# Performance work log

Measured on AMD Instinct MI355X. Metric: run time of the kernel, lower is better.

Reference implementation:

```python
import jax, jax.numpy as jnp
import numpy as np

SCALES = (4, 8, 8)
PAD = 2
TOTAL = 256  # prod(SCALES) == frame shift
INDENT = PAD * TOTAL
BN_EPS = 1e-3  # keras BatchNormalization default


def _bn(x, g, b, m, v):
    return (x - m) * jax.lax.rsqrt(v + BN_EPS) * g + b


def _conv1d_valid(x, w):
    # x: [B, T, Cin], w: [K, Cin, Cout]
    return jax.lax.conv_general_dilated(x, w, (1,), 'VALID',
                                         dimension_numbers=('NWC', 'WIO', 'NWC'))


def _mel_conv_same(x, w):
    # per-mel-bin shared 1D conv along time. x: [B, T, M], w: [K]
    B, T, M = x.shape
    lhs = x.transpose(0, 2, 1).reshape(B * M, T, 1)
    rhs = w.reshape(-1, 1, 1)
    y = jax.lax.conv_general_dilated(lhs, rhs, (1,), 'SAME',
                                     dimension_numbers=('NWC', 'WIO', 'NWC'))
    return y.reshape(B, M, T).transpose(0, 2, 1)


def _gru(x, Wx, Wh, bx, bh):
    # keras GRUCell (reset_after=True): gate order z, r, h; h' = z*h + (1-z)*hh
    xp = x @ Wx + bx  # [B, T, 3H], input projection hoisted out of the scan
    H = Wh.shape[0]
    h0 = jnp.zeros((x.shape[0], H), x.dtype)

    def step(h, xt):
        rp = h @ Wh + bh
        xz, xr, xh = jnp.split(xt, 3, axis=-1)
        rz, rr, rh = jnp.split(rp, 3, axis=-1)
        z = jax.nn.sigmoid(xz + rz)
        r = jax.nn.sigmoid(xr + rr)
        hh = jnp.tanh(xh + r * rh)
        hn = z * h + (1.0 - z) * hh
        return hn, hn

    _, ys = jax.lax.scan(step, h0, xp.transpose(1, 0, 2))
    return ys.transpose(1, 0, 2)


def setup_inputs() -> dict:
    key = jax.random.key(0)
    ks = iter(jax.random.split(key, 64))
    B, T_MEL, M, C, H, R = 4, 44, 80, 128, 512, 10
    T_UP = TOTAL * (T_MEL - 2 * PAD)  # 10240
    s = 0.05
    d = {}
    d['audios'] = jax.random.normal(next(ks), (B, T_UP + 1), jnp.float32)
    d['mels'] = jax.random.normal(next(ks), (B, T_MEL, M), jnp.float32)
    d['w_mel0'] = jnp.full((2 * SCALES[0] + 1,), 1.0 / (2 * SCALES[0] + 1), jnp.float32)
    d['w_mel1'] = jnp.full((2 * SCALES[1] + 1,), 1.0 / (2 * SCALES[1] + 1), jnp.float32)
    d['w_mel2'] = jnp.full((2 * SCALES[2] + 1,), 1.0 / (2 * SCALES[2] + 1), jnp.float32)
    d['mr_conv0_w'] = jax.random.normal(next(ks), (5, M, C), jnp.float32) * s
    d['mr_bn0_g'] = jax.random.uniform(next(ks), (C,), jnp.float32, 0.5, 1.5)
    d['mr_bn0_b'] = jax.random.normal(next(ks), (C,), jnp.float32) * s
    d['mr_bn0_m'] = jnp.zeros((C,), jnp.float32)
    d['mr_bn0_v'] = jnp.ones((C,), jnp.float32)
    d['r_w1'] = jax.random.normal(next(ks), (R, C, C), jnp.float32) * s
    d['r_bn1_g'] = jax.random.uniform(next(ks), (R, C), jnp.float32, 0.5, 1.5)
    d['r_bn1_b'] = jax.random.normal(next(ks), (R, C), jnp.float32) * s
    d['r_bn1_m'] = jnp.zeros((R, C), jnp.float32)
    d['r_bn1_v'] = jnp.ones((R, C), jnp.float32)
    d['r_w2'] = jax.random.normal(next(ks), (R, C, C), jnp.float32) * s
    d['r_bn2_g'] = jax.random.uniform(next(ks), (R, C), jnp.float32, 0.5, 1.5)
    d['r_bn2_b'] = jax.random.normal(next(ks), (R, C), jnp.float32) * s
    d['r_bn2_m'] = jnp.zeros((R, C), jnp.float32)
    d['r_bn2_v'] = jnp.ones((R, C), jnp.float32)
    d['mr_out_w'] = jax.random.normal(next(ks), (C, C), jnp.float32) * s
    d['mr_out_b'] = jnp.zeros((C,), jnp.float32)
    A4 = C // 4  # 32
    d['Wi'] = jax.random.normal(next(ks), (1 + M + A4, H), jnp.float32) * s
    d['bi'] = jnp.zeros((H,), jnp.float32)
    d['Wx0'] = jax.random.normal(next(ks), (H, 3 * H), jnp.float32) * s
    d['Wh0'] = jax.random.normal(next(ks), (H, 3 * H), jnp.float32) * s
    d['bx0'] = jnp.zeros((3 * H,), jnp.float32)
    d['bh0'] = jnp.zeros((3 * H,), jnp.float32)
    d['Wx1'] = jax.random.normal(next(ks), (H + A4, 3 * H), jnp.float32) * s
    d['Wh1'] = jax.random.normal(next(ks), (H, 3 * H), jnp.float32) * s
    d['bx1'] = jnp.zeros((3 * H,), jnp.float32)
    d['bh1'] = jnp.zeros((3 * H,), jnp.float32)
    d['Wd0'] = jax.random.normal(next(ks), (H + A4, H), jnp.float32) * s
    d['bd0'] = jnp.zeros((H,), jnp.float32)
    d['Wd1'] = jax.random.normal(next(ks), (H + A4, H), jnp.float32) * s
    d['bd1'] = jnp.zeros((H,), jnp.float32)
    d['Wp'] = jax.random.normal(next(ks), (H, 30), jnp.float32) * s
    d['bp'] = jnp.zeros((30,), jnp.float32)
    return d


def reference(audios, mels, w_mel0, w_mel1, w_mel2,
              mr_conv0_w, mr_bn0_g, mr_bn0_b, mr_bn0_m, mr_bn0_v,
              r_w1, r_bn1_g, r_bn1_b, r_bn1_m, r_bn1_v,
              r_w2, r_bn2_g, r_bn2_b, r_bn2_m, r_bn2_v,
              mr_out_w, mr_out_b, Wi, bi,
              Wx0, Wh0, bx0, bh0, Wx1, Wh1, bx1, bh1,
              Wd0, bd0, Wd1, bd1, Wp, bp):
    # ---- UpsampleNet mel branch: nearest upsample + smoothing conv per scale ----
    x = mels
    for w, scale in zip((w_mel0, w_mel1, w_mel2), SCALES):
        x = jnp.repeat(x, scale, axis=1)
        x = _mel_conv_same(x, w)
    mels_up = x[:, INDENT:-INDENT, :]  # [B, T_up, 80]

    # ---- UpsampleNet aux branch: MelResNet (inference BN) + nearest upsample ----
    a = jax.nn.relu(_bn(_conv1d_valid(mels, mr_conv0_w),
                        mr_bn0_g, mr_bn0_b, mr_bn0_m, mr_bn0_v))
    for i in range(r_w1.shape[0]):
        y = jax.nn.relu(_bn(a @ r_w1[i], r_bn1_g[i], r_bn1_b[i], r_bn1_m[i], r_bn1_v[i]))
        y = _bn(y @ r_w2[i], r_bn2_g[i], r_bn2_b[i], r_bn2_m[i], r_bn2_v[i])
        a = a + y
    a = a @ mr_out_w + mr_out_b
    aux = jnp.repeat(a, TOTAL, axis=1)  # [B, T_up, 128]
    a0, a1, a2, a3 = jnp.split(aux, 4, axis=-1)

    # ---- WaveRNN teacher-forced trunk ----
    x = jnp.concatenate([audios[:, :-1, None], mels_up, a0], axis=-1)
    x = x @ Wi + bi  # [B, T_up, 512]
    x = _gru(x, Wx0, Wh0, bx0, bh0) + x
    x = _gru(jnp.concatenate([x, a1], axis=-1), Wx1, Wh1, bx1, bh1) + x
    x = jax.nn.relu(jnp.concatenate([x, a2], axis=-1) @ Wd0 + bd0) + x
    x = jax.nn.relu(jnp.concatenate([x, a3], axis=-1) @ Wd1 + bd1) + x
    logits = x @ Wp + bp  # [B, T_up, 30] (MoL parameters)
    return logits
```

## Files before the change

kernel.cpp:

```cpp
#include <hip/hip_runtime.h>
#include <hip/hip_bf16.h>

#define T_SEQ 10240
#define GRU_W 8

typedef short bf16x8 __attribute__((ext_vector_type(8)));
typedef float f32x4 __attribute__((ext_vector_type(4)));

__device__ __forceinline__ float bf2f(unsigned short u) {
    return __uint_as_float(((unsigned int)u) << 16);
}

__global__ void upsample_kernel(const float* __restrict__ in, float* __restrict__ out,
                                const float* __restrict__ wk,
                                int B, int Tin, int Tout, int shift, int taps)
{
    int idx = blockIdx.x * blockDim.x + threadIdx.x;
    int total = B * Tout * 80;
    if (idx >= total) return;
    int m = idx % 80;
    int r = idx / 80;
    int t = r % Tout;
    int b = r / Tout;
    int s = taps >> 1;
    float acc = 0.f;
    for (int d = -s; d <= s; ++d) {
        int i = t + d;
        if (i >= 0 && i < Tout)
            acc += in[((size_t)b * Tin + (i >> shift)) * 80 + m] * wk[d + s];
    }
    out[idx] = acc;
}

__global__ __launch_bounds__(128) void conv0_kernel(
    const float* __restrict__ mels, const float* __restrict__ w,
    const float* __restrict__ g, const float* __restrict__ b,
    const float* __restrict__ m_, const float* __restrict__ v_,
    float* __restrict__ a)
{
    __shared__ float xin[400];
    int bt = blockIdx.x;
    int bb = bt / 40, t = bt % 40;
    int c = threadIdx.x;
    for (int idx = c; idx < 400; idx += 128)
        xin[idx] = mels[((size_t)bb * 44 + t + idx / 80) * 80 + (idx % 80)];
    __syncthreads();
    float s = 0.f;
    for (int q = 0; q < 400; ++q) s += xin[q] * w[q * 128 + c];
    s = (s - m_[c]) * rsqrtf(v_[c] + 1e-3f) * g[c] + b[c];
    a[bt * 128 + c] = fmaxf(s, 0.f);
}

__global__ __launch_bounds__(128) void resblock_kernel(
    const float* __restrict__ W1, const float* __restrict__ W2,
    const float* __restrict__ g1, const float* __restrict__ b1,
    const float* __restrict__ m1, const float* __restrict__ v1,
    const float* __restrict__ g2, const float* __restrict__ b2,
    const float* __restrict__ m2, const float* __restrict__ v2,
    float* __restrict__ a)
{
    __shared__ float ain[128], y1[128];
    int tok = blockIdx.x;
    int c = threadIdx.x;
    ain[c] = a[tok * 128 + c];
    __syncthreads();
    float s = 0.f;
    #pragma unroll 8
    for (int k = 0; k < 128; ++k) s += ain[k] * W1[k * 128 + c];
    s = (s - m1[c]) * rsqrtf(v1[c] + 1e-3f) * g1[c] + b1[c];
    y1[c] = fmaxf(s, 0.f);
    __syncthreads();
    float s2 = 0.f;
    #pragma unroll 8
    for (int k = 0; k < 128; ++k) s2 += y1[k] * W2[k * 128 + c];
    s2 = (s2 - m2[c]) * rsqrtf(v2[c] + 1e-3f) * g2[c] + b2[c];
    a[tok * 128 + c] = ain[c] + s2;
}

__global__ __launch_bounds__(128) void outmat_kernel(
    const float* __restrict__ W, const float* __restrict__ bias,
    const float* __restrict__ a, float* __restrict__ out)
{
    __shared__ float ain[128];
    int tok = blockIdx.x;
    int c = threadIdx.x;
    ain[c] = a[tok * 128 + c];
    __syncthreads();
    float s = 0.f;
    #pragma unroll 8
    for (int k = 0; k < 128; ++k) s += ain[k] * W[k * 128 + c];
    out[tok * 128 + c] = s + bias[c];
}

__device__ __forceinline__ float fetchA(int mode, int row, int k, int K,
    const float* audio, const float* melsup, const float* cond, const float* xA)
{
    if (k >= K) return 0.f;
    int b = row / T_SEQ;
    int t = row - b * T_SEQ;
    if (mode == 0) {
        if (k == 0) return audio[(size_t)b * (T_SEQ + 1) + t];
        if (k < 81) return melsup[((size_t)b * 11264 + 512 + t) * 80 + (k - 1)];
        return cond[((size_t)b * 40 + (t >> 8)) * 128 + (k - 81)];
    }
    if (k < 512) return xA[(size_t)row * 512 + k];
    int co = (mode == 2) ? 32 : (mode == 3) ? 64 : 96;
    return cond[((size_t)b * 40 + (t >> 8)) * 128 + co + (k - 512)];
}

__global__ __launch_bounds__(256) void gemm_big(
    int mode, int N, int K,
    const float* __restrict__ W, const float* __restrict__ bias1,
    const float* __restrict__ bias2,
    const float* __restrict__ audio, const float* __restrict__ melsup,
    const float* __restrict__ cond, const float* __restrict__ xA,
    const float* __restrict__ resid, float* __restrict__ outF,
    __hip_bfloat16* __restrict__ outB)
{
    __shared__ float As[16][68];
    __shared__ float Bs[16][68];
    const int tid = threadIdx.x;
    const int row0 = blockIdx.y * 64;
    const int col0 = blockIdx.x * 64;
    const int tx = tid & 15, ty = tid >> 4;
    float acc[4][4] = {};
    const int nkt = (K + 15) >> 4;
    for (int kt = 0; kt < nkt; ++kt) {
        const int kb = kt << 4;
        #pragma unroll
        for (int l = 0; l < 4; ++l) {
            int k = (tid >> 6) + l * 4;
            int m = tid & 63;
            float bv = 0.f;
            if (kb + k < K) bv = W[(size_t)(kb + k) * N + col0 + m];
            Bs[k][m] = bv;
        }
        if (mode != 0) {
            int m = tid >> 2, kq = tid & 3;
            int row = row0 + m;
            int k = kb + kq * 4;
            if (k + 3 < 512) {
                float4 v = *reinterpret_cast<const float4*>(xA + (size_t)row * 512 + k);
                As[kq * 4 + 0][m] = v.x; As[kq * 4 + 1][m] = v.y;
                As[kq * 4 + 2][m] = v.z; As[kq * 4 + 3][m] = v.w;
            } else {
                #pragma unroll
                for (int i = 0; i < 4; ++i)
                    As[kq * 4 + i][m] = fetchA(mode, row, k + i, K, audio, melsup, cond, xA);
            }
        } else {
            #pragma unroll
            for (int l = 0; l < 4; ++l) {
                int k = (tid >> 6) + l * 4;
                int m = tid & 63;
                As[k][m] = fetchA(0, row0 + m, kb + k, K, audio, melsup, cond, xA);
            }
        }
        __syncthreads();
        #pragma unroll
        for (int k = 0; k < 16; ++k) {
            float a0 = As[k][(ty << 2) + 0], a1 = As[k][(ty << 2) + 1];
            float a2 = As[k][(ty << 2) + 2], a3 = As[k][(ty << 2) + 3];
            float b0 = Bs[k][(tx << 2) + 0], b1 = Bs[k][(tx << 2) + 1];
            float b2 = Bs[k][(tx << 2) + 2], b3 = Bs[k][(tx << 2) + 3];
            acc[0][0] += a0 * b0; acc[0][1] += a0 * b1; acc[0][2] += a0 * b2; acc[0][3] += a0 * b3;
            acc[1][0] += a1 * b0; acc[1][1] += a1 * b1; acc[1][2] += a1 * b2; acc[1][3] += a1 * b3;
            acc[2][0] += a2 * b0; acc[2][1] += a2 * b1; acc[2][2] += a2 * b2; acc[2][3] += a2 * b3;
            acc[3][0] += a3 * b0; acc[3][1] += a3 * b1; acc[3][2] += a3 * b2; acc[3][3] += a3 * b3;
        }
        __syncthreads();
    }
    #pragma unroll
    for (int i = 0; i < 4; ++i) {
        int row = row0 + (ty << 2) + i;
        #pragma unroll
        for (int jt = 0; jt < 4; ++jt) {
            int col = col0 + (tx << 2) + jt;
            float v = acc[i][jt] + bias1[col];
            if (bias2 && col < 1024) v += bias2[col];
            if (mode == 0) {
                outF[(size_t)row * N + col] = v;
            } else if (mode <= 2) {
                outB[(size_t)row * 1536 + col] = __float2bfloat16(v);
            } else {
                v = fmaxf(v, 0.f) + resid[(size_t)row * 512 + col];
                outF[(size_t)row * 512 + col] = v;
            }
        }
    }
}

__global__ __launch_bounds__(256) void pack_wh_kernel(const float* __restrict__ Wh,
                                                      unsigned short* __restrict__ out)
{
    int gid = blockIdx.x * 256 + threadIdx.x;
    int l = gid & 63;
    int idx = gid >> 6;
    int kt = idx & 15; idx >>= 4;
    int ntL = idx & 1; idx >>= 1;
    int w = idx % 6;
    int wg = idx / 6;
    int nt = 2 * w + ntL;
    int g = nt >> 2, u = nt & 3;
    int n = g * 512 + wg * 64 + u * 16 + (l & 15);
    int k0 = kt * 32 + (l >> 4) * 8;
    unsigned short* dst = out + (size_t)gid * 8;
    #pragma unroll
    for (int i = 0; i < 8; ++i) {
        __hip_bfloat16 hv = __float2bfloat16(Wh[(size_t)(k0 + i) * 1536 + n]);
        dst[i] = *reinterpret_cast<unsigned short*>(&hv);
    }
}

__global__ __launch_bounds__(512, 2) void gru_mfma8(
    const unsigned short* __restrict__ wpack,
    const float* __restrict__ bh,
    const __hip_bfloat16* __restrict__ xp,
    float* __restrict__ xio,
    unsigned int* __restrict__ hpair,
    int T)
{
    __shared__ alignas(16) unsigned short h_sh[16 * 512];
    __shared__ alignas(16) unsigned short xp_sh[2][4][3][64];
    __shared__ alignas(8)  float xv_sh[2][4][64];
    __shared__ alignas(16) float acc_sh[12][16][4];

    const int tid = threadIdx.x;
    const int wg = blockIdx.x;
    const int w = tid >> 6;
    const int l = tid & 63;

    {
        uint4* z = reinterpret_cast<uint4*>(h_sh);
        z[tid] = make_uint4(0, 0, 0, 0);
        z[tid + 512] = make_uint4(0, 0, 0, 0);
    }

    bf16x8 wf[2][16];
    if (w < 6) {
        const bf16x8* wp = reinterpret_cast<const bf16x8*>(wpack);
        const int base = (wg * 6 + w) * 2 * 16 * 64;
        #pragma unroll
        for (int n = 0; n < 2; ++n)
            #pragma unroll
            for (int kt = 0; kt < 16; ++kt)
                wf[n][kt] = wp[base + (n * 16 + kt) * 64 + l];
    }

    float bhh = 0.f, hprev = 0.f;
    if (tid < 256) bhh = bh[1024 + wg * 64 + (tid & 63)];

    if (tid < 128) {
        for (int z = tid; z < 192; z += 128) {
            int bg = z >> 4, s = z & 15;
            int b = bg / 3, g = bg % 3;
            unsigned long long v = *reinterpret_cast<const unsigned long long*>(
                reinterpret_cast<const unsigned short*>(xp) +
                (size_t)(b * T) * 1536 + g * 512 + wg * 64 + s * 4);
            *reinterpret_cast<unsigned long long*>(&xp_sh[0][b][g][s * 4]) = v;
        }
        int b = tid >> 5, pr = tid & 31;
        float2 v = *reinterpret_cast<const float2*>(
            xio + (size_t)(b * T) * 512 + wg * 64 + pr * 2);
        *reinterpret_cast<float2*>(&xv_sh[0][b][pr * 2]) = v;
    }
    __syncthreads();

    const unsigned long long* hp64 = reinterpret_cast<const unsigned long long*>(hpair);

    for (int t = 0; t < T; ++t) {
        const int cur = t & 1, nxt = cur ^ 1;

        const unsigned long long* src = hp64 + (size_t)cur * 1024 + tid * 2;
        const unsigned tg = (unsigned)t & 0xffffu;
        unsigned long long u0 = __hip_atomic_load(src + 0, __ATOMIC_RELAXED, __HIP_MEMORY_SCOPE_AGENT);
        unsigned long long u1 = __hip_atomic_load(src + 1, __ATOMIC_RELAXED, __HIP_MEMORY_SCOPE_AGENT);
        while ((((unsigned)(u0 >> 16) & 0xffffu) != tg) | ((unsigned)(u0 >> 48) != tg) |
               (((unsigned)(u1 >> 16) & 0xffffu) != tg) | ((unsigned)(u1 >> 48) != tg)) {
            __builtin_amdgcn_s_sleep(1);
            u0 = __hip_atomic_load(src + 0, __ATOMIC_RELAXED, __HIP_MEMORY_SCOPE_AGENT);
            u1 = __hip_atomic_load(src + 1, __ATOMIC_RELAXED, __HIP_MEMORY_SCOPE_AGENT);
        }
        {
            const int pb = tid >> 7;
            const int j0 = (tid * 4) & 511;
            unsigned long long wv =
                (u0 & 0xffffull) | ((u0 >> 32) & 0xffffull) << 16 |
                (u1 & 0xffffull) << 32 | ((u1 >> 32) & 0xffffull) << 48;
            const int chunk = (j0 >> 3) ^ (pb & 7);
            *reinterpret_cast<unsigned long long*>(
                reinterpret_cast<char*>(h_sh) + pb * 1024 + chunk * 16 + (j0 & 7) * 2) = wv;
        }
        __syncthreads();

        if (w >= 6 && t + 1 < T) {
            int t6 = tid - 384;
            for (int z = t6; z < 192; z += 128) {
                int bg = z >> 4, s = z & 15;
                int b = bg / 3, g = bg % 3;
                unsigned long long v = *reinterpret_cast<const unsigned long long*>(
                    reinterpret_cast<const unsigned short*>(xp) +
                    (size_t)(b * T + t + 1) * 1536 + g * 512 + wg * 64 + s * 4);
                *reinterpret_cast<unsigned long long*>(&xp_sh[nxt][b][g][s * 4]) = v;
            }
            int b = t6 >> 5, pr = t6 & 31;
            float2 v = *reinterpret_cast<const float2*>(
                xio + (size_t)(b * T + t + 1) * 512 + wg * 64 + pr * 2);
            *reinterpret_cast<float2*>(&xv_sh[nxt][b][pr * 2]) = v;
        }

        if (w < 6) {
            f32x4 acc0 = {0, 0, 0, 0}, acc1 = {0, 0, 0, 0};
            const int rb = l & 15, q = l >> 4;
            #pragma unroll
            for (int kt = 0; kt < 16; ++kt) {
                bf16x8 afr = *reinterpret_cast<const bf16x8*>(
                    reinterpret_cast<const char*>(h_sh) + rb * 1024 +
                    ((((kt * 4 + q) ^ (rb & 7))) << 4));
                acc0 = __builtin_amdgcn_mfma_f32_16x16x32_bf16(afr, wf[0][kt], acc0, 0, 0, 0);
                acc1 = __builtin_amdgcn_mfma_f32_16x16x32_bf16(afr, wf[1][kt], acc1, 0, 0, 0);
            }
            if (l < 16) {
                *reinterpret_cast<f32x4*>(&acc_sh[2 * w][l][0]) = acc0;
                *reinterpret_cast<f32x4*>(&acc_sh[2 * w + 1][l][0]) = acc1;
            }
        }
        __syncthreads();

        if (tid < 256) {
            const int b = tid >> 6, jl = tid & 63, j = wg * 64 + jl;
            const int u = jl >> 4, n16 = jl & 15;
            float az = acc_sh[u][n16][b];
            float ar = acc_sh[4 + u][n16][b];
            float ah = acc_sh[8 + u][n16][b];
            float xz = bf2f(xp_sh[cur][b][0][jl]);
            float xr = bf2f(xp_sh[cur][b][1][jl]);
            float xh = bf2f(xp_sh[cur][b][2][jl]);
            float xv = xv_sh[cur][b][jl];
            float z = 1.f / (1.f + __expf(-(xz + az)));
            float r = 1.f / (1.f + __expf(-(xr + ar)));
            float e2 = __expf(-2.f * (xh + r * (ah + bhh)));
            float hh = (1.f - e2) / (1.f + e2);
            float hn = z * hprev + (1.f - z) * hh;
            hprev = hn;
            __hip_bfloat16 hb16 = __float2bfloat16(hn);
            unsigned hv = ((unsigned)((t + 1) & 0xffff) << 16) |
                          (unsigned)*reinterpret_cast<unsigned short*>(&hb16);
            __hip_atomic_store(hpair + (size_t)nxt * 2048 + b * 512 + j, hv,
                               __ATOMIC_RELAXED, __HIP_MEMORY_SCOPE_AGENT);
            xio[(size_t)(b * T + t) * 512 + j] = xv + hn;
        }
    }
}

__global__ __launch_bounds__(256) void wp_kernel(
    const float* __restrict__ x, const float* __restrict__ Wp,
    const float* __restrict__ bp, float* __restrict__ out)
{
    int r = threadIdx.x >> 5, c = threadIdx.x & 31;
    size_t row = (size_t)blockIdx.x * 8 + r;
    if (c >= 30) return;
    const float* xr = x + row * 512;
    float acc = 0.f;
    #pragma unroll 8
    for (int k = 0; k < 512; ++k) acc += xr[k] * Wp[k * 30 + c];
    out[row * 30 + c] = acc + bp[c];
}

extern "C" void kernel_launch(void* const* d_in, const int* in_sizes, int n_in,
                              void* d_out, int out_size, void* d_ws, size_t ws_size,
                              hipStream_t stream)
{
    const float* audios = (const float*)d_in[0];
    const float* mels   = (const float*)d_in[1];
    const float* w_mel0 = (const float*)d_in[2];
    const float* w_mel1 = (const float*)d_in[3];
    const float* w_mel2 = (const float*)d_in[4];
    const float* conv0w = (const float*)d_in[5];
    const float* bn0g = (const float*)d_in[6];
    const float* bn0b = (const float*)d_in[7];
    const float* bn0m = (const float*)d_in[8];
    const float* bn0v = (const float*)d_in[9];
    const float* r_w1   = (const float*)d_in[10];
    const float* r_bn1g = (const float*)d_in[11];
    const float* r_bn1b = (const float*)d_in[12];
    const float* r_bn1m = (const float*)d_in[13];
    const float* r_bn1v = (const float*)d_in[14];
    const float* r_w2   = (const float*)d_in[15];
    const float* r_bn2g = (const float*)d_in[16];
    const float* r_bn2b = (const float*)d_in[17];
    const float* r_bn2m = (const float*)d_in[18];
    const float* r_bn2v = (const float*)d_in[19];
    const float* mr_out_w = (const float*)d_in[20];
    const float* mr_out_b = (const float*)d_in[21];
    const float* Wi = (const float*)d_in[22];
    const float* bi = (const float*)d_in[23];
    const float* Wx0 = (const float*)d_in[24];
    const float* Wh0 = (const float*)d_in[25];
    const float* bx0 = (const float*)d_in[26];
    const float* bh0 = (const float*)d_in[27];
    const float* Wx1 = (const float*)d_in[28];
    const float* Wh1 = (const float*)d_in[29];
    const float* bx1 = (const float*)d_in[30];
    const float* bh1 = (const float*)d_in[31];
    const float* Wd0 = (const float*)d_in[32];
    const float* bd0 = (const float*)d_in[33];
    const float* Wd1 = (const float*)d_in[34];
    const float* bd1 = (const float*)d_in[35];
    const float* Wp = (const float*)d_in[36];
    const float* bp = (const float*)d_in[37];

    char* ws = (char*)d_ws;
    size_t off = 0;
    auto alloc = [&](size_t n) { size_t r = off; off += (n + 255) & ~(size_t)255; return r; };
    const size_t M = 4 * (size_t)T_SEQ;
    size_t xp_off = alloc(M * 1536 * 2);
    size_t x_off  = alloc(M * 512 * 4);
    size_t s1_off = alloc((size_t)4 * 176 * 80 * 4);
    size_t s2_off = alloc((size_t)4 * 1408 * 80 * 4);
    size_t s3_off = alloc((size_t)4 * 11264 * 80 * 4);
    size_t ca_off = alloc((size_t)160 * 128 * 4);
    size_t cf_off = alloc((size_t)160 * 128 * 4);
    size_t wp0_off = alloc((size_t)98304 * 8 * 2);
    size_t wp1_off = alloc((size_t)98304 * 8 * 2);
    size_t hp_off  = alloc(2 * 2048 * 4);

    __hip_bfloat16* xp = (__hip_bfloat16*)(ws + xp_off);
    float* x3   = (float*)(ws + xp_off);
    float* xbuf = (float*)(ws + x_off);
    float* st1  = (float*)(ws + s1_off);
    float* st2  = (float*)(ws + s2_off);
    float* st3  = (float*)(ws + s3_off);
    float* conda = (float*)(ws + ca_off);
    float* condf = (float*)(ws + cf_off);
    unsigned short* wpack0 = (unsigned short*)(ws + wp0_off);
    unsigned short* wpack1 = (unsigned short*)(ws + wp1_off);
    unsigned int* hpair = (unsigned int*)(ws + hp_off);
    float* outp = (float*)d_out;

    pack_wh_kernel<<<384, 256, 0, stream>>>(Wh0, wpack0);
    pack_wh_kernel<<<384, 256, 0, stream>>>(Wh1, wpack1);

    {
        int tot1 = 4 * 176 * 80;
        upsample_kernel<<<(tot1 + 255) / 256, 256, 0, stream>>>(mels, st1, w_mel0, 4, 44, 176, 2, 9);
        int tot2 = 4 * 1408 * 80;
        upsample_kernel<<<(tot2 + 255) / 256, 256, 0, stream>>>(st1, st2, w_mel1, 4, 176, 1408, 3, 17);
        int tot3 = 4 * 11264 * 80;
        upsample_kernel<<<(tot3 + 255) / 256, 256, 0, stream>>>(st2, st3, w_mel2, 4, 1408, 11264, 3, 17);
    }
    conv0_kernel<<<160, 128, 0, stream>>>(mels, conv0w, bn0g, bn0b, bn0m, bn0v, conda);
    for (int i = 0; i < 10; ++i) {
        resblock_kernel<<<160, 128, 0, stream>>>(
            r_w1 + (size_t)i * 128 * 128, r_w2 + (size_t)i * 128 * 128,
            r_bn1g + i * 128, r_bn1b + i * 128, r_bn1m + i * 128, r_bn1v + i * 128,
            r_bn2g + i * 128, r_bn2b + i * 128, r_bn2m + i * 128, r_bn2v + i * 128,
            conda);
    }
    outmat_kernel<<<160, 128, 0, stream>>>(mr_out_w, mr_out_b, conda, condf);

    dim3 blk(256);
    gemm_big<<<dim3(8, 640), blk, 0, stream>>>(0, 512, 113, Wi, bi, nullptr,
        audios, st3, condf, nullptr, nullptr, xbuf, nullptr);
    gemm_big<<<dim3(24, 640), blk, 0, stream>>>(1, 1536, 512, Wx0, bx0, bh0,
        nullptr, nullptr, condf, xbuf, nullptr, nullptr, xp);
    hipMemsetAsync(ws + hp_off, 0, 2 * 2048 * 4, stream);
    gru_mfma8<<<GRU_W, 512, 0, stream>>>(wpack0, bh0, xp, xbuf, hpair, T_SEQ);
    gemm_big<<<dim3(24, 640), blk, 0, stream>>>(2, 1536, 544, Wx1, bx1, bh1,
        nullptr, nullptr, condf, xbuf, nullptr, nullptr, xp);
    hipMemsetAsync(ws + hp_off, 0, 2 * 2048 * 4, stream);
    gru_mfma8<<<GRU_W, 512, 0, stream>>>(wpack1, bh1, xp, xbuf, hpair, T_SEQ);
    gemm_big<<<dim3(8, 640), blk, 0, stream>>>(3, 512, 544, Wd0, bd0, nullptr,
        nullptr, nullptr, condf, xbuf, xbuf, x3, nullptr);
    gemm_big<<<dim3(8, 640), blk, 0, stream>>>(4, 512, 544, Wd1, bd1, nullptr,
        nullptr, nullptr, condf, x3, x3, xbuf, nullptr);
    wp_kernel<<<5120, 256, 0, stream>>>(xbuf, Wp, bp, outp);
}
```

Before: 47.59 ms.

## Move dense GEMMs to bf16 MFMA and deepen GRU input staging pipeline

Replaces the fp32 SIMT GEMM for the GRU input projections and the two dense layers with a bf16 MFMA kernel that uses pre-transposed, padded bf16 weight copies. The goal is to cut the time spent in these large matmuls. The GRU recurrence kernel also changes: it uses a 3-slot staging buffer with a register-held prefetch two steps ahead, and 16-byte hidden-state polling loads done by half of the threads. The trade-offs are extra bf16 rounding of the activations and weights, plus more packing kernels at startup.

```diff
diff --git a/kernel.cpp b/kernel.cpp
--- a/kernel.cpp
+++ b/kernel.cpp
@@ -9,6 +9,10 @@
 
 __device__ __forceinline__ float bf2f(unsigned short u) {
     return __uint_as_float(((unsigned int)u) << 16);
+}
+__device__ __forceinline__ unsigned short f2bf(float f) {
+    __hip_bfloat16 h = __float2bfloat16(f);
+    return *reinterpret_cast<unsigned short*>(&h);
 }
 
 __global__ void upsample_kernel(const float* __restrict__ in, float* __restrict__ out,
@@ -92,30 +96,11 @@
     out[tok * 128 + c] = s + bias[c];
 }
 
-__device__ __forceinline__ float fetchA(int mode, int row, int k, int K,
-    const float* audio, const float* melsup, const float* cond, const float* xA)
-{
-    if (k >= K) return 0.f;
-    int b = row / T_SEQ;
-    int t = row - b * T_SEQ;
-    if (mode == 0) {
-        if (k == 0) return audio[(size_t)b * (T_SEQ + 1) + t];
-        if (k < 81) return melsup[((size_t)b * 11264 + 512 + t) * 80 + (k - 1)];
-        return cond[((size_t)b * 40 + (t >> 8)) * 128 + (k - 81)];
-    }
-    if (k < 512) return xA[(size_t)row * 512 + k];
-    int co = (mode == 2) ? 32 : (mode == 3) ? 64 : 96;
-    return cond[((size_t)b * 40 + (t >> 8)) * 128 + co + (k - 512)];
-}
-
 __global__ __launch_bounds__(256) void gemm_big(
-    int mode, int N, int K,
+    int N, int K,
     const float* __restrict__ W, const float* __restrict__ bias1,
-    const float* __restrict__ bias2,
     const float* __restrict__ audio, const float* __restrict__ melsup,
-    const float* __restrict__ cond, const float* __restrict__ xA,
-    const float* __restrict__ resid, float* __restrict__ outF,
-    __hip_bfloat16* __restrict__ outB)
+    const float* __restrict__ cond, float* __restrict__ outF)
 {
     __shared__ float As[16][68];
     __shared__ float Bs[16][68];
@@ -134,27 +119,17 @@
             float bv = 0.f;
             if (kb + k < K) bv = W[(size_t)(kb + k) * N + col0 + m];
             Bs[k][m] = bv;
-        }
-        if (mode != 0) {
-            int m = tid >> 2, kq = tid & 3;
             int row = row0 + m;
-            int k = kb + kq * 4;
-            if (k + 3 < 512) {
-                float4 v = *reinterpret_cast<const float4*>(xA + (size_t)row * 512 + k);
-                As[kq * 4 + 0][m] = v.x; As[kq * 4 + 1][m] = v.y;
-                As[kq * 4 + 2][m] = v.z; As[kq * 4 + 3][m] = v.w;
-            } else {
-                #pragma unroll
-                for (int i = 0; i < 4; ++i)
-                    As[kq * 4 + i][m] = fetchA(mode, row, k + i, K, audio, melsup, cond, xA);
-            }
-        } else {
-            #pragma unroll
-            for (int l = 0; l < 4; ++l) {
-                int k = (tid >> 6) + l * 4;
-                int m = tid & 63;
-                As[k][m] = fetchA(0, row0 + m, kb + k, K, audio, melsup, cond, xA);
-            }
+            int b = row / T_SEQ;
+            int t = row - b * T_SEQ;
+            int kk = kb + k;
+            float av = 0.f;
+            if (kk < K) {
+                if (kk == 0) av = audio[(size_t)b * (T_SEQ + 1) + t];
+                else if (kk < 81) av = melsup[((size_t)b * 11264 + 512 + t) * 80 + (kk - 1)];
+                else av = cond[((size_t)b * 40 + (t >> 8)) * 128 + (kk - 81)];
+            }
+            As[k][m] = av;
         }
         __syncthreads();
         #pragma unroll
@@ -176,15 +151,120 @@
         #pragma unroll
         for (int jt = 0; jt < 4; ++jt) {
             int col = col0 + (tx << 2) + jt;
-            float v = acc[i][jt] + bias1[col];
-            if (bias2 && col < 1024) v += bias2[col];
-            if (mode == 0) {
-                outF[(size_t)row * N + col] = v;
-            } else if (mode <= 2) {
-                outB[(size_t)row * 1536 + col] = __float2bfloat16(v);
+            outF[(size_t)row * N + col] = acc[i][jt] + bias1[col];
+        }
+    }
+}
+
+__global__ __launch_bounds__(256) void pack_wt_kernel(const float* __restrict__ W,
+                                                      unsigned short* __restrict__ out,
+                                                      int K, int N)
+{
+    int idx = blockIdx.x * 256 + threadIdx.x;
+    if (idx >= N * 576) return;
+    int n = idx / 576, kp = idx % 576;
+    out[idx] = (kp < K) ? f2bf(W[(size_t)kp * N + n]) : (unsigned short)0;
+}
+
+__global__ __launch_bounds__(256) void gemm_mfma(
+    int mode, int K,
+    const unsigned short* __restrict__ Wt,
+    const float* __restrict__ bias1,
+    const float* __restrict__ bias2,
+    const float* __restrict__ cond,
+    const float* __restrict__ xA,
+    const float* __restrict__ resid,
+    float* __restrict__ outF,
+    __hip_bfloat16* __restrict__ outB)
+{
+    __shared__ alignas(16) unsigned short A_sh[64][72];
+    __shared__ alignas(16) unsigned short B_sh[128][72];
+    const int tid = threadIdx.x;
+    const int row0 = blockIdx.y * 64;
+    const int col0 = blockIdx.x * 128;
+    const int wv = tid >> 6, l = tid & 63;
+
+    f32x4 acc[4][2] = {};
+    const int nkt = (K + 63) >> 6;
+    for (int it = 0; it < nkt; ++it) {
+        const int kb = it << 6;
+        {
+            const int r = tid >> 2, q = tid & 3;
+            const int row = row0 + r;
+            unsigned short tmp[16];
+            if (kb + 64 <= 512) {
+                const float* src = xA + (size_t)row * 512 + kb + q * 16;
+                #pragma unroll
+                for (int e = 0; e < 16; e += 4) {
+                    float4 v = *reinterpret_cast<const float4*>(src + e);
+                    tmp[e + 0] = f2bf(v.x); tmp[e + 1] = f2bf(v.y);
+                    tmp[e + 2] = f2bf(v.z); tmp[e + 3] = f2bf(v.w);
+                }
             } else {
-                v = fmaxf(v, 0.f) + resid[(size_t)row * 512 + col];
-                outF[(size_t)row * 512 + col] = v;
+                const int b = row / T_SEQ, trow = row - b * T_SEQ;
+                const int co = (mode == 2) ? 32 : (mode == 3) ? 64 : 96;
+                const float* cp = cond + ((size_t)b * 40 + (trow >> 8)) * 128 + co;
+                #pragma unroll
+                for (int e = 0; e < 16; ++e) {
+                    int k = kb + q * 16 + e;
+                    float v = 0.f;
+                    if (k < 512) v = xA[(size_t)row * 512 + k];
+                    else if (k < K) v = cp[k - 512];
+                    tmp[e] = f2bf(v);
+                }
+            }
+            #pragma unroll
+            for (int e = 0; e < 16; e += 8)
+                *reinterpret_cast<uint4*>(&A_sh[r][q * 16 + e]) =
+                    *reinterpret_cast<const uint4*>(&tmp[e]);
+        }
+        {
+            const int c = tid >> 1, half = tid & 1;
+            const unsigned short* src = Wt + (size_t)(col0 + c) * 576 + kb + half * 32;
+            #pragma unroll
+            for (int e = 0; e < 32; e += 8)
+                *reinterpret_cast<uint4*>(&B_sh[c][half * 32 + e]) =
+                    *reinterpret_cast<const uint4*>(src + e);
+        }
+        __syncthreads();
+        const int rsel = l & 15, q = l >> 4;
+        #pragma unroll
+        for (int ks = 0; ks < 2; ++ks) {
+            bf16x8 a[4], b[2];
+            #pragma unroll
+            for (int mf = 0; mf < 4; ++mf)
+                a[mf] = *reinterpret_cast<const bf16x8*>(
+                    &A_sh[mf * 16 + rsel][ks * 32 + q * 8]);
+            #pragma unroll
+            for (int nf = 0; nf < 2; ++nf)
+                b[nf] = *reinterpret_cast<const bf16x8*>(
+                    &B_sh[wv * 32 + nf * 16 + rsel][ks * 32 + q * 8]);
+            #pragma unroll
+            for (int mf = 0; mf < 4; ++mf)
+                #pragma unroll
+                for (int nf = 0; nf < 2; ++nf)
+                    acc[mf][nf] = __builtin_amdgcn_mfma_f32_16x16x32_bf16(
+                        a[mf], b[nf], acc[mf][nf], 0, 0, 0);
+        }
+        __syncthreads();
+    }
+    const int rsel = l & 15, q = l >> 4;
+    #pragma unroll
+    for (int mf = 0; mf < 4; ++mf) {
+        #pragma unroll
+        for (int nf = 0; nf < 2; ++nf) {
+            #pragma unroll
+            for (int i = 0; i < 4; ++i) {
+                int row = row0 + mf * 16 + q * 4 + i;
+                int col = col0 + wv * 32 + nf * 16 + rsel;
+                float v = acc[mf][nf][i] + bias1[col];
+                if (mode <= 2) {
+                    if (col < 1024) v += bias2[col];
+                    outB[(size_t)row * 1536 + col] = __float2bfloat16(v);
+                } else {
+                    v = fmaxf(v, 0.f) + resid[(size_t)row * 512 + col];
+                    outF[(size_t)row * 512 + col] = v;
+                }
             }
         }
     }
@@ -206,10 +286,8 @@
     int k0 = kt * 32 + (l >> 4) * 8;
     unsigned short* dst = out + (size_t)gid * 8;
     #pragma unroll
-    for (int i = 0; i < 8; ++i) {
-        __hip_bfloat16 hv = __float2bfloat16(Wh[(size_t)(k0 + i) * 1536 + n]);
-        dst[i] = *reinterpret_cast<unsigned short*>(&hv);
-    }
+    for (int i = 0; i < 8; ++i)
+        dst[i] = f2bf(Wh[(size_t)(k0 + i) * 1536 + n]);
 }
 
 __global__ __launch_bounds__(512, 2) void gru_mfma8(
@@ -221,8 +299,8 @@
     int T)
 {
     __shared__ alignas(16) unsigned short h_sh[16 * 512];
-    __shared__ alignas(16) unsigned short xp_sh[2][4][3][64];
-    __shared__ alignas(8)  float xv_sh[2][4][64];
+    __shared__ alignas(16) unsigned short xp_sh[3][4][3][64];
+    __shared__ alignas(16) float xv_sh[3][4][64];
     __shared__ alignas(16) float acc_sh[12][16][4];
 
     const int tid = threadIdx.x;
@@ -232,8 +310,7 @@
 
     {
         uint4* z = reinterpret_cast<uint4*>(h_sh);
-        z[tid] = make_uint4(0, 0, 0, 0);
-        z[tid + 512] = make_uint4(0, 0, 0, 0);
+        for (int i = tid; i < 1024; i += 512) z[i] = make_uint4(0, 0, 0, 0);
     }
 
     bf16x8 wf[2][16];
@@ -250,64 +327,79 @@
     float bhh = 0.f, hprev = 0.f;
     if (tid < 256) bhh = bh[1024 + wg * 64 + (tid & 63)];
 
-    if (tid < 128) {
-        for (int z = tid; z < 192; z += 128) {
-            int bg = z >> 4, s = z & 15;
-            int b = bg / 3, g = bg % 3;
-            unsigned long long v = *reinterpret_cast<const unsigned long long*>(
-                reinterpret_cast<const unsigned short*>(xp) +
-                (size_t)(b * T) * 1536 + g * 512 + wg * 64 + s * 4);
-            *reinterpret_cast<unsigned long long*>(&xp_sh[0][b][g][s * 4]) = v;
-        }
-        int b = tid >> 5, pr = tid & 31;
-        float2 v = *reinterpret_cast<const float2*>(
-            xio + (size_t)(b * T) * 512 + wg * 64 + pr * 2);
-        *reinterpret_cast<float2*>(&xv_sh[0][b][pr * 2]) = v;
+    const int xc = tid - 384;
+    uint4 hold_a = make_uint4(0, 0, 0, 0), hold_b = make_uint4(0, 0, 0, 0);
+    #define STAGE_LOAD(c, t, dstv)                                              \
+        { int c_ = (c);                                                         \
+          if (c_ < 96) { int g_ = c_ / 32, b_ = (c_ % 32) / 8, s_ = c_ % 8;     \
+            dstv = *reinterpret_cast<const uint4*>(                             \
+                reinterpret_cast<const unsigned short*>(xp) +                   \
+                ((size_t)b_ * T + (t)) * 1536 + g_ * 512 + wg * 64 + s_ * 8);   \
+          } else { int d_ = c_ - 96, b_ = d_ >> 4, s_ = d_ & 15;                \
+            dstv = *reinterpret_cast<const uint4*>(                             \
+                xio + ((size_t)b_ * T + (t)) * 512 + wg * 64 + s_ * 4); } }
+    #define STAGE_WRITE(c, buf, v)                                              \
+        { int c_ = (c);                                                         \
+          if (c_ < 96) { int g_ = c_ / 32, b_ = (c_ % 32) / 8, s_ = c_ % 8;     \
+            *reinterpret_cast<uint4*>(&xp_sh[buf][b_][g_][s_ * 8]) = v;         \
+          } else { int d_ = c_ - 96, b_ = d_ >> 4, s_ = d_ & 15;                \
+            *reinterpret_cast<uint4*>(&xv_sh[buf][b_][s_ * 4]) = v; } }
+
+    if (w >= 6) {
+        uint4 v;
+        STAGE_LOAD(xc, 0, v); STAGE_WRITE(xc, 0, v);
+        if (xc < 32) { STAGE_LOAD(128 + xc, 0, v); STAGE_WRITE(128 + xc, 0, v); }
+        if (T > 1) {
+            STAGE_LOAD(xc, 1, hold_a);
+            if (xc < 32) STAGE_LOAD(128 + xc, 1, hold_b);
+        }
     }
     __syncthreads();
 
     const unsigned long long* hp64 = reinterpret_cast<const unsigned long long*>(hpair);
+    const int pb = tid >> 6;
+    const int pchunk = (tid & 63) ^ (pb & 7);
 
     for (int t = 0; t < T; ++t) {
-        const int cur = t & 1, nxt = cur ^ 1;
-
-        const unsigned long long* src = hp64 + (size_t)cur * 1024 + tid * 2;
-        const unsigned tg = (unsigned)t & 0xffffu;
-        unsigned long long u0 = __hip_atomic_load(src + 0, __ATOMIC_RELAXED, __HIP_MEMORY_SCOPE_AGENT);
-        unsigned long long u1 = __hip_atomic_load(src + 1, __ATOMIC_RELAXED, __HIP_MEMORY_SCOPE_AGENT);
-        while ((((unsigned)(u0 >> 16) & 0xffffu) != tg) | ((unsigned)(u0 >> 48) != tg) |
-               (((unsigned)(u1 >> 16) & 0xffffu) != tg) | ((unsigned)(u1 >> 48) != tg)) {
-            __builtin_amdgcn_s_sleep(1);
-            u0 = __hip_atomic_load(src + 0, __ATOMIC_RELAXED, __HIP_MEMORY_SCOPE_AGENT);
-            u1 = __hip_atomic_load(src + 1, __ATOMIC_RELAXED, __HIP_MEMORY_SCOPE_AGENT);
-        }
-        {
-            const int pb = tid >> 7;
-            const int j0 = (tid * 4) & 511;
-            unsigned long long wv =
-                (u0 & 0xffffull) | ((u0 >> 32) & 0xffffull) << 16 |
-                (u1 & 0xffffull) << 32 | ((u1 >> 32) & 0xffffull) << 48;
-            const int chunk = (j0 >> 3) ^ (pb & 7);
-            *reinterpret_cast<unsigned long long*>(
-                reinterpret_cast<char*>(h_sh) + pb * 1024 + chunk * 16 + (j0 & 7) * 2) = wv;
+        const int cur = t & 1;
+        const int bu = t % 3;
+
+        if (tid < 256) {
+            const unsigned long long* src = hp64 + (size_t)cur * 1024 + tid * 4;
+            const unsigned tg = (unsigned)t & 0xffffu;
+            unsigned long long u0 = __hip_atomic_load(src + 0, __ATOMIC_RELAXED, __HIP_MEMORY_SCOPE_AGENT);
+            unsigned long long u1 = __hip_atomic_load(src + 1, __ATOMIC_RELAXED, __HIP_MEMORY_SCOPE_AGENT);
+            unsigned long long u2 = __hip_atomic_load(src + 2, __ATOMIC_RELAXED, __HIP_MEMORY_SCOPE_AGENT);
+            unsigned long long u3 = __hip_atomic_load(src + 3, __ATOMIC_RELAXED, __HIP_MEMORY_SCOPE_AGENT);
+            while ((((unsigned)(u0 >> 16) & 0xffffu) != tg) | ((unsigned)(u0 >> 48) != tg) |
+                   (((unsigned)(u1 >> 16) & 0xffffu) != tg) | ((unsigned)(u1 >> 48) != tg) |
+                   (((unsigned)(u2 >> 16) & 0xffffu) != tg) | ((unsigned)(u2 >> 48) != tg) |
+                   (((unsigned)(u3 >> 16) & 0xffffu) != tg) | ((unsigned)(u3 >> 48) != tg)) {
+                __builtin_amdgcn_s_sleep(1);
+                u0 = __hip_atomic_load(src + 0, __ATOMIC_RELAXED, __HIP_MEMORY_SCOPE_AGENT);
+                u1 = __hip_atomic_load(src + 1, __ATOMIC_RELAXED, __HIP_MEMORY_SCOPE_AGENT);
+                u2 = __hip_atomic_load(src + 2, __ATOMIC_RELAXED, __HIP_MEMORY_SCOPE_AGENT);
+                u3 = __hip_atomic_load(src + 3, __ATOMIC_RELAXED, __HIP_MEMORY_SCOPE_AGENT);
+            }
+            uint4 wv;
+            wv.x = (unsigned)(u0 & 0xffffull) | ((unsigned)((u0 >> 32) & 0xffffull) << 16);
+            wv.y = (unsigned)(u1 & 0xffffull) | ((unsigned)((u1 >> 32) & 0xffffull) << 16);
+            wv.z = (unsigned)(u2 & 0xffffull) | ((unsigned)((u2 >> 32) & 0xffffull) << 16);
+            wv.w = (unsigned)(u3 & 0xffffull) | ((unsigned)((u3 >> 32) & 0xffffull) << 16);
+            *reinterpret_cast<uint4*>(
+                reinterpret_cast<char*>(h_sh) + pb * 1024 + pchunk * 16) = wv;
+        } else if (w >= 6) {
+            if (t + 1 < T) {
+                const int bn = (t + 1) % 3;
+                STAGE_WRITE(xc, bn, hold_a);
+                if (xc < 32) STAGE_WRITE(128 + xc, bn, hold_b);
+            }
+            if (t + 2 < T) {
+                STAGE_LOAD(xc, t + 2, hold_a);
+                if (xc < 32) STAGE_LOAD(128 + xc, t + 2, hold_b);
+            }
         }
         __syncthreads();
-
-        if (w >= 6 && t + 1 < T) {
-            int t6 = tid - 384;
-            for (int z = t6; z < 192; z += 128) {
-                int bg = z >> 4, s = z & 15;
-                int b = bg / 3, g = bg % 3;
-                unsigned long long v = *reinterpret_cast<const unsigned long long*>(
-                    reinterpret_cast<const unsigned short*>(xp) +
-                    (size_t)(b * T + t + 1) * 1536 + g * 512 + wg * 64 + s * 4);
-                *reinterpret_cast<unsigned long long*>(&xp_sh[nxt][b][g][s * 4]) = v;
-            }
-            int b = t6 >> 5, pr = t6 & 31;
-            float2 v = *reinterpret_cast<const float2*>(
-                xio + (size_t)(b * T + t + 1) * 512 + wg * 64 + pr * 2);
-            *reinterpret_cast<float2*>(&xv_sh[nxt][b][pr * 2]) = v;
-        }
 
         if (w < 6) {
             f32x4 acc0 = {0, 0, 0, 0}, acc1 = {0, 0, 0, 0};
@@ -333,24 +425,24 @@
             float az = acc_sh[u][n16][b];
             float ar = acc_sh[4 + u][n16][b];
             float ah = acc_sh[8 + u][n16][b];
-            float xz = bf2f(xp_sh[cur][b][0][jl]);
-            float xr = bf2f(xp_sh[cur][b][1][jl]);
-            float xh = bf2f(xp_sh[cur][b][2][jl]);
-            float xv = xv_sh[cur][b][jl];
+            float xz = bf2f(xp_sh[bu][b][0][jl]);
+            float xr = bf2f(xp_sh[bu][b][1][jl]);
+            float xh = bf2f(xp_sh[bu][b][2][jl]);
+            float xv = xv_sh[bu][b][jl];
             float z = 1.f / (1.f + __expf(-(xz + az)));
             float r = 1.f / (1.f + __expf(-(xr + ar)));
             float e2 = __expf(-2.f * (xh + r * (ah + bhh)));
             float hh = (1.f - e2) / (1.f + e2);
             float hn = z * hprev + (1.f - z) * hh;
             hprev = hn;
-            __hip_bfloat16 hb16 = __float2bfloat16(hn);
-            unsigned hv = ((unsigned)((t + 1) & 0xffff) << 16) |
-                          (unsigned)*reinterpret_cast<unsigned short*>(&hb16);
-            __hip_atomic_store(hpair + (size_t)nxt * 2048 + b * 512 + j, hv,
+            unsigned hv = ((unsigned)((t + 1) & 0xffff) << 16) | (unsigned)f2bf(hn);
+            __hip_atomic_store(hpair + (size_t)((t + 1) & 1) * 2048 + b * 512 + j, hv,
                                __ATOMIC_RELAXED, __HIP_MEMORY_SCOPE_AGENT);
-            xio[(size_t)(b * T + t) * 512 + j] = xv + hn;
-        }
-    }
+            xio[((size_t)b * T + t) * 512 + j] = xv + hn;
+        }
+    }
+    #undef STAGE_LOAD
+    #undef STAGE_WRITE
 }
 
 __global__ __launch_bounds__(256) void wp_kernel(
@@ -423,6 +515,10 @@
     size_t cf_off = alloc((size_t)160 * 128 * 4);
     size_t wp0_off = alloc((size_t)98304 * 8 * 2);
     size_t wp1_off = alloc((size_t)98304 * 8 * 2);
+    size_t wt1_off = alloc((size_t)1536 * 576 * 2);
+    size_t wt2_off = alloc((size_t)1536 * 576 * 2);
+    size_t wt3_off = alloc((size_t)512 * 576 * 2);
+    size_t wt4_off = alloc((size_t)512 * 576 * 2);
     size_t hp_off  = alloc(2 * 2048 * 4);
 
     __hip_bfloat16* xp = (__hip_bfloat16*)(ws + xp_off);
@@ -435,20 +531,24 @@
     float* condf = (float*)(ws + cf_off);
     unsigned short* wpack0 = (unsigned short*)(ws + wp0_off);
     unsigned short* wpack1 = (unsigned short*)(ws + wp1_off);
+    unsigned short* wt1 = (unsigned short*)(ws + wt1_off);
+    unsigned short* wt2 = (unsigned short*)(ws + wt2_off);
+    unsigned short* wt3 = (unsigned short*)(ws + wt3_off);
+    unsigned short* wt4 = (unsigned short*)(ws + wt4_off);
     unsigned int* hpair = (unsigned int*)(ws + hp_off);
     float* outp = (float*)d_out;
 
     pack_wh_kernel<<<384, 256, 0, stream>>>(Wh0, wpack0);
     pack_wh_kernel<<<384, 256, 0, stream>>>(Wh1, wpack1);
-
-    {
-        int tot1 = 4 * 176 * 80;
-        upsample_kernel<<<(tot1 + 255) / 256, 256, 0, stream>>>(mels, st1, w_mel0, 4, 44, 176, 2, 9);
-        int tot2 = 4 * 1408 * 80;
-        upsample_kernel<<<(tot2 + 255) / 256, 256, 0, stream>>>(st1, st2, w_mel1, 4, 176, 1408, 3, 17);
-        int tot3 = 4 * 11264 * 80;
-        upsample_kernel<<<(tot3 + 255) / 256, 256, 0, stream>>>(st2, st3, w_mel2, 4, 1408, 11264, 3, 17);
-    }
+    pack_wt_kernel<<<(1536 * 576 + 255) / 256, 256, 0, stream>>>(Wx0, wt1, 512, 1536);
+    pack_wt_kernel<<<(1536 * 576 + 255) / 256, 256, 0, stream>>>(Wx1, wt2, 544, 1536);
+    pack_wt_kernel<<<(512 * 576 + 255) / 256, 256, 0, stream>>>(Wd0, wt3, 544, 512);
+    pack_wt_kernel<<<(512 * 576 + 255) / 256, 256, 0, stream>>>(Wd1, wt4, 544, 512);
+
+    upsample_kernel<<<(4 * 176 * 80 + 255) / 256, 256, 0, stream>>>(mels, st1, w_mel0, 4, 44, 176, 2, 9);
+    upsample_kernel<<<(4 * 1408 * 80 + 255) / 256, 256, 0, stream>>>(st1, st2, w_mel1, 4, 176, 1408, 3, 17);
+    upsample_kernel<<<(4 * 11264 * 80 + 255) / 256, 256, 0, stream>>>(st2, st3, w_mel2, 4, 1408, 11264, 3, 17);
+
     conv0_kernel<<<160, 128, 0, stream>>>(mels, conv0w, bn0g, bn0b, bn0m, bn0v, conda);
     for (int i = 0; i < 10; ++i) {
         resblock_kernel<<<160, 128, 0, stream>>>(
@@ -459,20 +559,19 @@
     }
     outmat_kernel<<<160, 128, 0, stream>>>(mr_out_w, mr_out_b, conda, condf);
 
-    dim3 blk(256);
-    gemm_big<<<dim3(8, 640), blk, 0, stream>>>(0, 512, 113, Wi, bi, nullptr,
-        audios, st3, condf, nullptr, nullptr, xbuf, nullptr);
-    gemm_big<<<dim3(24, 640), blk, 0, stream>>>(1, 1536, 512, Wx0, bx0, bh0,
-        nullptr, nullptr, condf, xbuf, nullptr, nullptr, xp);
+    gemm_big<<<dim3(8, 640), 256, 0, stream>>>(512, 113, Wi, bi, audios, st3, condf, xbuf);
+
+    gemm_mfma<<<dim3(12, 640), 256, 0, stream>>>(1, 512, wt1, bx0, bh0, condf,
+        xbuf, nullptr, nullptr, xp);
     hipMemsetAsync(ws + hp_off, 0, 2 * 2048 * 4, stream);
     gru_mfma8<<<GRU_W, 512, 0, stream>>>(wpack0, bh0, xp, xbuf, hpair, T_SEQ);
-    gemm_big<<<dim3(24, 640), blk, 0, stream>>>(2, 1536, 544, Wx1, bx1, bh1,
-        nullptr, nullptr, condf, xbuf, nullptr, nullptr, xp);
+    gemm_mfma<<<dim3(12, 640), 256, 0, stream>>>(2, 544, wt2, bx1, bh1, condf,
+        xbuf, nullptr, nullptr, xp);
     hipMemsetAsync(ws + hp_off, 0, 2 * 2048 * 4, stream);
     gru_mfma8<<<GRU_W, 512, 0, stream>>>(wpack1, bh1, xp, xbuf, hpair, T_SEQ);
-    gemm_big<<<dim3(8, 640), blk, 0, stream>>>(3, 512, 544, Wd0, bd0, nullptr,
-        nullptr, nullptr, condf, xbuf, xbuf, x3, nullptr);
-    gemm_big<<<dim3(8, 640), blk, 0, stream>>>(4, 512, 544, Wd1, bd1, nullptr,
-        nullptr, nullptr, condf, x3, x3, xbuf, nullptr);
+    gemm_mfma<<<dim3(4, 640), 256, 0, stream>>>(3, 544, wt3, bd0, nullptr, condf,
+        xbuf, xbuf, x3, nullptr);
+    gemm_mfma<<<dim3(4, 640), 256, 0, stream>>>(4, 544, wt4, bd1, nullptr, condf,
+        x3, x3, xbuf, nullptr);
     wp_kernel<<<5120, 256, 0, stream>>>(xbuf, Wp, bp, outp);
 }
```

Result: faster. 39.80 ms (median of 2 runs) (-16.4%).
